# Optimization experiments

Hardware: AMD Instinct MI355X
Metric: run time of the kernel (lower is better)

## Reference

```python
import jax, jax.numpy as jnp
import numpy as np

N = 50000       # nodes
E = 1600000     # edges (avg degree 32)
F_IN = 128      # input node features
HID = 64        # hidden_dim
H = 2           # heads in conv1
NEG_SLOPE = 0.2 # PyG GATConv default


def gat_conv(x, W, a_src, a_dst, b, src, dst, heads, out_ch):
    """PyG-style GATConv (concat=True). x:[n,f], W:[f,heads*out_ch],
    a_src/a_dst:[heads,out_ch], b:[heads*out_ch], src/dst:[e]."""
    n = x.shape[0]
    xh = (x @ W).reshape(n, heads, out_ch)              # [n,H,C]
    s_src = jnp.sum(xh * a_src[None], axis=-1)          # [n,H]
    s_dst = jnp.sum(xh * a_dst[None], axis=-1)          # [n,H]
    e = jax.nn.leaky_relu(s_src[src] + s_dst[dst], NEG_SLOPE)  # [e,H]
    # segment softmax over incoming edges of each destination node
    emax = jax.ops.segment_max(e, dst, num_segments=n)  # [n,H]
    emax = jnp.where(jnp.isfinite(emax), emax, 0.0)
    p = jnp.exp(e - emax[dst])
    denom = jax.ops.segment_sum(p, dst, num_segments=n)
    alpha = p / (denom[dst] + 1e-16)                    # [e,H]
    out = jax.ops.segment_sum(xh[src] * alpha[..., None], dst, num_segments=n)
    return out.reshape(n, heads * out_ch) + b


def setup_inputs() -> dict:
    key = jax.random.key(0)
    ks = jax.random.split(key, 14)
    g = lambda k, shape, fan: jax.random.normal(k, shape, jnp.float32) / np.sqrt(fan).astype(np.float32)
    return {
        "x": jax.random.normal(ks[0], (N, F_IN), jnp.float32),
        "edge_index": jax.random.randint(ks[1], (2, E), 0, N, jnp.int32),
        "W1": g(ks[2], (F_IN, H * HID), F_IN),
        "a_src1": g(ks[3], (H, HID), HID),
        "a_dst1": g(ks[4], (H, HID), HID),
        "b1": jnp.zeros((H * HID,), jnp.float32),
        "W2": g(ks[5], (H * HID, HID), H * HID),
        "a_src2": g(ks[6], (1, HID), HID),
        "a_dst2": g(ks[7], (1, HID), HID),
        "b2": jnp.zeros((HID,), jnp.float32),
        "Wm": g(ks[8], (HID, 1), HID),
        "bm": jnp.zeros((1,), jnp.float32),
        "Wl": g(ks[9], (HID, 4), HID),
        "bl": jnp.zeros((4,), jnp.float32),
    }


def reference(x, edge_index, W1, a_src1, a_dst1, b1, W2, a_src2, a_dst2, b2, Wm, bm, Wl, bl):
    n = x.shape[0]
    loop = jnp.arange(n, dtype=edge_index.dtype)        # PyG add_self_loops=True
    src = jnp.concatenate([edge_index[0], loop])
    dst = jnp.concatenate([edge_index[1], loop])
    h = jax.nn.relu(gat_conv(x, W1, a_src1, a_dst1, b1, src, dst, H, HID))
    # dropout layers are identity in eval mode
    h = jax.nn.relu(gat_conv(h, W2, a_src2, a_dst2, b2, src, dst, 1, HID))
    mortality = h @ Wm + bm   # [n,1]
    los = h @ Wl + bl         # [n,4]
    return (mortality, los)
```

## Files before the change

kernel.cpp:

```cpp
#include <hip/hip_runtime.h>
#include <hip/hip_bf16.h>

typedef __hip_bfloat16 bf16;
typedef __attribute__((ext_vector_type(8))) short short8;
typedef __attribute__((ext_vector_type(4))) float f32x4;

static __device__ __forceinline__ float b2f(const bf16 v){ return __bfloat162float(v); }
static __device__ __forceinline__ float lrelu(float x){ return x > 0.f ? x : 0.2f * x; }

static __device__ __forceinline__ float ldf(const void* p, size_t i, int f32){
  return f32 ? ((const float*)p)[i] : __bfloat162float(((const bf16*)p)[i]);
}

static __device__ __forceinline__ float wsum(float v){
#pragma unroll
  for (int o = 32; o; o >>= 1) v += __shfl_xor(v, o, 64);
  return v;
}
static __device__ __forceinline__ float qsum(float v){
  v += __shfl_xor(v, 1); v += __shfl_xor(v, 2);
  v += __shfl_xor(v, 4); v += __shfl_xor(v, 8);
  return v;
}

static __device__ __forceinline__ unsigned short f2bf(float x){
  unsigned u = __float_as_uint(x);
  unsigned r = (u + 0x7fffu + ((u >> 16) & 1u)) >> 16;
  return (unsigned short)r;
}
static __device__ __forceinline__ float bfval(unsigned short h){
  return __uint_as_float(((unsigned)h) << 16);
}
static __device__ __forceinline__ unsigned packbf2(float a, float b){
  return ((unsigned)f2bf(b) << 16) | (unsigned)f2bf(a);
}
static __device__ __forceinline__ float unlo(unsigned v){ return __uint_as_float(v << 16); }
static __device__ __forceinline__ float unhi(unsigned v){ return __uint_as_float(v & 0xffff0000u); }

__global__ void k_detect(const unsigned short* __restrict__ x, int* __restrict__ flag,
                         int* __restrict__ bucketCur, int nbuck){
  __shared__ int cnt;
  if (threadIdx.x == 0) cnt = 0;
  __syncthreads();
  int bad = 0;
  for (int i = threadIdx.x; i < 8192; i += 256){
    int e = (x[i] >> 7) & 0xFF;
    if (e >= 133) bad++;
  }
  atomicAdd(&cnt, bad);
  for (int i = threadIdx.x; i < nbuck; i += 256) bucketCur[i] = 0;
  __syncthreads();
  if (threadIdx.x == 0) *flag = (cnt > 16) ? 1 : 0;
}

#define CAP 10240
#define EPB 16
#define CHUNK (256 * EPB)

__global__ __launch_bounds__(256) void k_binscatter(const int* __restrict__ ei,
                                                    int* __restrict__ bucketCur,
                                                    unsigned* __restrict__ binned,
                                                    int E, int Etot){
  __shared__ int lcnt[256];
  __shared__ int lcur[256];
  int t = threadIdx.x;
  lcnt[t] = 0;
  __syncthreads();
  int base = blockIdx.x * CHUNK;
  int vsrc[EPB], vdst[EPB];
#pragma unroll
  for (int k = 0; k < EPB; k++){
    int i = base + k * 256 + t;
    vdst[k] = -1;
    if (i < Etot){
      if (i < E){ vsrc[k] = ei[i]; vdst[k] = ei[E + i]; }
      else { vsrc[k] = i - E; vdst[k] = i - E; }
      atomicAdd(&lcnt[vdst[k] >> 8], 1);
    }
  }
  __syncthreads();
  lcur[t] = lcnt[t] ? atomicAdd(&bucketCur[t], lcnt[t]) : 0;
  __syncthreads();
#pragma unroll
  for (int k = 0; k < EPB; k++){
    if (vdst[k] >= 0){
      int b = vdst[k] >> 8;
      int p = atomicAdd(&lcur[b], 1);
      binned[(size_t)b * CAP + p] = (unsigned)vsrc[k] | ((unsigned)(vdst[k] & 255) << 24);
    }
  }
}

#define SORTCAP 10240
__global__ __launch_bounds__(256) void k_bucketsort(const int* __restrict__ bucketCur,
                                                    const unsigned* __restrict__ binned,
                                                    int* __restrict__ deg, int* __restrict__ offs,
                                                    int* __restrict__ csr, int N){
  __shared__ int lcnt[256];
  __shared__ int lsc[256];
  __shared__ int lcur[256];
  __shared__ int lsrc[SORTCAP];
  int t = threadIdx.x;
  int b = blockIdx.x;
  int s0 = b * CAP;
  int cnt = bucketCur[b];
  int node0 = b << 8;
  lcnt[t] = 0;
  __syncthreads();
  for (int i = t; i < cnt; i += 256){
    unsigned v = binned[s0 + i];
    atomicAdd(&lcnt[v >> 24], 1);
  }
  __syncthreads();
  lsc[t] = lcnt[t];
  __syncthreads();
#pragma unroll
  for (int o = 1; o < 256; o <<= 1){
    int x = (t >= o) ? lsc[t - o] : 0;
    __syncthreads();
    lsc[t] += x;
    __syncthreads();
  }
  int excl = lsc[t] - lcnt[t];
  int node = node0 + t;
  if (node < N){ deg[node] = lcnt[t]; offs[node] = s0 + excl; }
  lcur[t] = excl;
  __syncthreads();
  if (cnt <= SORTCAP){
    for (int i = t; i < cnt; i += 256){
      unsigned v = binned[s0 + i];
      int p = atomicAdd(&lcur[v >> 24], 1);
      lsrc[p] = (int)(v & 0xFFFFFFu);
    }
    __syncthreads();
    for (int i = t; i < cnt; i += 256) csr[s0 + i] = lsrc[i];
  } else {
    for (int i = t; i < cnt; i += 256){
      unsigned v = binned[s0 + i];
      int p = atomicAdd(&lcur[v >> 24], 1);
      csr[s0 + p] = (int)(v & 0xFFFFFFu);
    }
  }
}

__global__ __launch_bounds__(256) void k_prepw2(const void* __restrict__ W1, const void* __restrict__ W2,
                                                const int* __restrict__ flagp,
                                                unsigned short* __restrict__ w1hi, unsigned short* __restrict__ w1lo,
                                                unsigned short* __restrict__ w2hi, unsigned short* __restrict__ w2lo){
  const int f = *flagp;
  int blk = blockIdx.x;
  const void* W; unsigned short *hi, *lo; int ncol, nct, t;
  if (blk < 64){ W = W1; hi = w1hi; lo = w1lo; ncol = 128; nct = 8; t = blk * 256 + threadIdx.x; }
  else         { W = W2; hi = w2hi; lo = w2lo; ncol = 64;  nct = 4; t = (blk - 64) * 256 + threadIdx.x; }
  int j = t & 7;
  int lane = (t >> 3) & 63;
  int ct = (t >> 9) % nct;
  int kc = t / (512 * nct);
  int k = kc * 32 + ((lane >> 4) << 3) + j;
  int col = ct * 16 + (lane & 15);
  float w = ldf(W, (size_t)k * ncol + col, f);
  unsigned short h = f2bf(w);
  hi[t] = h;
  lo[t] = f2bf(w - bfval(h));
}

__global__ __launch_bounds__(256) void k_gemm1m(
    const void* __restrict__ x,
    const unsigned short* __restrict__ whi, const unsigned short* __restrict__ wlo,
    const void* __restrict__ a_src1, const void* __restrict__ a_dst1,
    const int* __restrict__ flagp,
    unsigned* __restrict__ xh1p, float* __restrict__ ssrc1, float* __restrict__ sdst1, int n){
  const int f = *flagp;
  int t = threadIdx.x;
  int lane = t & 63, w = t >> 6;
  int c16 = lane & 15, quad = lane >> 4;
  int nbw = blockIdx.x * 64 + w * 16;
  int an = min(nbw + c16, n - 1);
  f32x4 acc[8];
#pragma unroll
  for (int ct = 0; ct < 8; ct++)
#pragma unroll
    for (int r = 0; r < 4; r++) acc[ct][r] = 0.f;

#pragma unroll
  for (int kc = 0; kc < 4; kc++){
    float av[8];
    short8 ahi, alo;
    if (f){
      const float* row = (const float*)x + (size_t)an * 128 + kc * 32 + quad * 8;
      float4 v0 = *(const float4*)row;
      float4 v1 = *(const float4*)(row + 4);
      av[0] = v0.x; av[1] = v0.y; av[2] = v0.z; av[3] = v0.w;
      av[4] = v1.x; av[5] = v1.y; av[6] = v1.z; av[7] = v1.w;
#pragma unroll
      for (int j = 0; j < 8; j++){
        unsigned short h = f2bf(av[j]);
        ahi[j] = (short)h;
        alo[j] = (short)f2bf(av[j] - bfval(h));
      }
    } else {
      const unsigned short* row = (const unsigned short*)x + (size_t)an * 128 + kc * 32 + quad * 8;
      uint4 v = *(const uint4*)row;
      ahi[0] = (short)(v.x & 0xffff); ahi[1] = (short)(v.x >> 16);
      ahi[2] = (short)(v.y & 0xffff); ahi[3] = (short)(v.y >> 16);
      ahi[4] = (short)(v.z & 0xffff); ahi[5] = (short)(v.z >> 16);
      ahi[6] = (short)(v.w & 0xffff); ahi[7] = (short)(v.w >> 16);
#pragma unroll
      for (int j = 0; j < 8; j++) alo[j] = 0;
    }
#pragma unroll
    for (int ct = 0; ct < 8; ct++){
      const short8 bhi = *(const short8*)(whi + (((size_t)(kc * 8 + ct) * 64 + lane) << 3));
      const short8 blo = *(const short8*)(wlo + (((size_t)(kc * 8 + ct) * 64 + lane) << 3));
      acc[ct] = __builtin_amdgcn_mfma_f32_16x16x32_bf16(ahi, blo, acc[ct], 0, 0, 0);
      acc[ct] = __builtin_amdgcn_mfma_f32_16x16x32_bf16(alo, bhi, acc[ct], 0, 0, 0);
      acc[ct] = __builtin_amdgcn_mfma_f32_16x16x32_bf16(ahi, bhi, acc[ct], 0, 0, 0);
    }
  }

  float as[8], ad[8];
#pragma unroll
  for (int ct = 0; ct < 8; ct++){
    as[ct] = ldf(a_src1, ct * 16 + c16, f);
    ad[ct] = ldf(a_dst1, ct * 16 + c16, f);
  }
  float vs0[4], vs1[4], vd0[4], vd1[4];
#pragma unroll
  for (int r = 0; r < 4; r++){
    float s0 = 0.f, s1 = 0.f, d0 = 0.f, d1 = 0.f;
#pragma unroll
    for (int ct = 0; ct < 4; ct++){
      s0 += acc[ct][r] * as[ct];      d0 += acc[ct][r] * ad[ct];
      s1 += acc[ct + 4][r] * as[ct + 4]; d1 += acc[ct + 4][r] * ad[ct + 4];
    }
    vs0[r] = qsum(s0); vs1[r] = qsum(s1);
    vd0[r] = qsum(d0); vd1[r] = qsum(d1);
  }
#pragma unroll
  for (int r = 0; r < 4; r++){
    int node = nbw + quad * 4 + r;
    if (node < n){
#pragma unroll
      for (int ct = 0; ct < 4; ct++)
        xh1p[(size_t)node * 64 + ct * 16 + c16] = packbf2(acc[ct][r], acc[ct + 4][r]);
    }
  }
  if (c16 == 0){
#pragma unroll
    for (int r = 0; r < 4; r++){
      int node = nbw + quad * 4 + r;
      if (node < n){
        ssrc1[node * 2]     = vs0[r];
        ssrc1[node * 2 + 1] = vs1[r];
        sdst1[node * 2]     = vd0[r];
        sdst1[node * 2 + 1] = vd1[r];
      }
    }
  }
}

__global__ __launch_bounds__(256) void k_gemm2m(
    const float* __restrict__ h1,
    const unsigned short* __restrict__ whi, const unsigned short* __restrict__ wlo,
    const void* __restrict__ a_src2, const void* __restrict__ a_dst2,
    const int* __restrict__ flagp,
    unsigned short* __restrict__ xh2b, float* __restrict__ ssrc2, float* __restrict__ sdst2, int n){
  const int f = *flagp;
  int t = threadIdx.x;
  int lane = t & 63, w = t >> 6;
  int c16 = lane & 15, quad = lane >> 4;
  int nbw = blockIdx.x * 64 + w * 16;
  int an = min(nbw + c16, n - 1);
  f32x4 acc[4];
#pragma unroll
  for (int ct = 0; ct < 4; ct++)
#pragma unroll
    for (int r = 0; r < 4; r++) acc[ct][r] = 0.f;

#pragma unroll
  for (int kc = 0; kc < 4; kc++){
    const float* row = h1 + (size_t)an * 128 + kc * 32 + quad * 8;
    float4 v0 = *(const float4*)row;
    float4 v1 = *(const float4*)(row + 4);
    float av[8] = {v0.x, v0.y, v0.z, v0.w, v1.x, v1.y, v1.z, v1.w};
    short8 ahi, alo;
#pragma unroll
    for (int j = 0; j < 8; j++){
      unsigned short h = f2bf(av[j]);
      ahi[j] = (short)h;
      alo[j] = (short)f2bf(av[j] - bfval(h));
    }
#pragma unroll
    for (int ct = 0; ct < 4; ct++){
      const short8 bhi = *(const short8*)(whi + (((size_t)(kc * 4 + ct) * 64 + lane) << 3));
      const short8 blo = *(const short8*)(wlo + (((size_t)(kc * 4 + ct) * 64 + lane) << 3));
      acc[ct] = __builtin_amdgcn_mfma_f32_16x16x32_bf16(ahi, blo, acc[ct], 0, 0, 0);
      acc[ct] = __builtin_amdgcn_mfma_f32_16x16x32_bf16(alo, bhi, acc[ct], 0, 0, 0);
      acc[ct] = __builtin_amdgcn_mfma_f32_16x16x32_bf16(ahi, bhi, acc[ct], 0, 0, 0);
    }
  }

  float as[4], ad[4];
#pragma unroll
  for (int ct = 0; ct < 4; ct++){
    as[ct] = ldf(a_src2, ct * 16 + c16, f);
    ad[ct] = ldf(a_dst2, ct * 16 + c16, f);
  }
  float vs[4], vd[4];
#pragma unroll
  for (int r = 0; r < 4; r++){
    float s = 0.f, d = 0.f;
#pragma unroll
    for (int ct = 0; ct < 4; ct++){
      s += acc[ct][r] * as[ct];
      d += acc[ct][r] * ad[ct];
    }
    vs[r] = qsum(s); vd[r] = qsum(d);
  }
#pragma unroll
  for (int r = 0; r < 4; r++){
    int node = nbw + quad * 4 + r;
    if (node < n){
#pragma unroll
      for (int ct = 0; ct < 4; ct++)
        xh2b[(size_t)node * 64 + ct * 16 + c16] = f2bf(acc[ct][r]);
    }
  }
  if (c16 == 0){
#pragma unroll
    for (int r = 0; r < 4; r++){
      int node = nbw + quad * 4 + r;
      if (node < n){ ssrc2[node] = vs[r]; sdst2[node] = vd[r]; }
    }
  }
}

__global__ __launch_bounds__(256) void k_agg1(
    const int* __restrict__ offs, const int* __restrict__ deg, const int* __restrict__ csr,
    const float2* __restrict__ ssrc, const float2* __restrict__ sdst,
    const unsigned* __restrict__ xh1p, const void* __restrict__ b1,
    const int* __restrict__ flagp, float* __restrict__ h1, int n){
  int wid = (int)(((size_t)blockIdx.x * blockDim.x + threadIdx.x) >> 6);
  int lane = threadIdx.x & 63;
  if (wid >= n) return;
  int st = offs[wid], d = deg[wid];
  int half = lane >> 5, u = lane & 31;
  float2 sd = sdst[wid];
  const uint2* xp = (const uint2*)xh1p;
  float Z0l = 0.f, Z1l = 0.f;
  float a0x = 0.f, a0y = 0.f, a1x = 0.f, a1y = 0.f;
  for (int base = 0; base < d; base += 64){
    int idx = base + lane;
    bool val = idx < d;
    int s = csr[st + (val ? idx : 0)];
    float2 sv = ssrc[s];
    float e0 = fminf(lrelu(sv.x + sd.x), 80.f);
    float e1 = fminf(lrelu(sv.y + sd.y), 80.f);
    float p0 = val ? __expf(e0) : 0.f;
    float p1 = val ? __expf(e1) : 0.f;
    Z0l += p0; Z1l += p1;
    int cnt = min(64, d - base);
    int pairs = (cnt + 1) >> 1;
    for (int pj = 0; pj < pairs; pj += 8){
      int sj[8]; float q0v[8], q1v[8]; uint2 vv[8];
#pragma unroll
      for (int k = 0; k < 8; k++){
        int jj = ((pj + k) << 1) + half;
        sj[k] = __shfl(s, jj);
        q0v[k] = __shfl(p0, jj);
        q1v[k] = __shfl(p1, jj);
      }
#pragma unroll
      for (int k = 0; k < 8; k++)
        vv[k] = xp[(size_t)(unsigned)sj[k] * 32 + u];
#pragma unroll
      for (int k = 0; k < 8; k++){
        a0x = fmaf(q0v[k], unlo(vv[k].x), a0x); a0y = fmaf(q0v[k], unlo(vv[k].y), a0y);
        a1x = fmaf(q1v[k], unhi(vv[k].x), a1x); a1y = fmaf(q1v[k], unhi(vv[k].y), a1y);
      }
    }
  }
  a0x += __shfl_xor(a0x, 32); a0y += __shfl_xor(a0y, 32);
  a1x += __shfl_xor(a1x, 32); a1y += __shfl_xor(a1y, 32);
  float Z0 = wsum(Z0l), Z1 = wsum(Z1l);
  const int f = *flagp;
  float Zh = half ? Z1 : Z0;
  float ax = half ? a1x : a0x;
  float ay = half ? a1y : a0y;
  float inv = 1.f / (Zh + 1e-16f);
  float bx = ldf(b1, half * 64 + 2 * u, f);
  float by = ldf(b1, half * 64 + 2 * u + 1, f);
  float2 o;
  o.x = fmaxf(ax * inv + bx, 0.f);
  o.y = fmaxf(ay * inv + by, 0.f);
  *(float2*)&h1[(size_t)wid * 128 + half * 64 + 2 * u] = o;
}

__global__ __launch_bounds__(256) void k_agg2(
    const int* __restrict__ offs, const int* __restrict__ deg, const int* __restrict__ csr,
    const float* __restrict__ ssrc, const float* __restrict__ sdstA,
    const unsigned short* __restrict__ xh2b, const void* __restrict__ bias2,
    const void* __restrict__ Wm, const void* __restrict__ bm,
    const void* __restrict__ Wlos, const void* __restrict__ bl,
    const int* __restrict__ flagp, void* __restrict__ out, int n){
  int wid = (int)(((size_t)blockIdx.x * blockDim.x + threadIdx.x) >> 6);
  int lane = threadIdx.x & 63;
  if (wid >= n) return;
  int st = offs[wid], d = deg[wid];
  int half = lane >> 5, u = lane & 31;
  float sd = sdstA[wid];
  const unsigned* xp = (const unsigned*)xh2b;
  float Zl = 0.f, ax = 0.f, ay = 0.f;
  for (int base = 0; base < d; base += 64){
    int idx = base + lane;
    bool val = idx < d;
    int s = csr[st + (val ? idx : 0)];
    float e = fminf(lrelu(ssrc[s] + sd), 80.f);
    float p = val ? __expf(e) : 0.f;
    Zl += p;
    int cnt = min(64, d - base);
    int pairs = (cnt + 1) >> 1;
    for (int pj = 0; pj < pairs; pj += 8){
      int sj[8]; float qv[8]; unsigned vv[8];
#pragma unroll
      for (int k = 0; k < 8; k++){
        int jj = ((pj + k) << 1) + half;
        sj[k] = __shfl(s, jj);
        qv[k] = __shfl(p, jj);
      }
#pragma unroll
      for (int k = 0; k < 8; k++)
        vv[k] = xp[(size_t)(unsigned)sj[k] * 32 + u];
#pragma unroll
      for (int k = 0; k < 8; k++){
        ax = fmaf(qv[k], unlo(vv[k]), ax);
        ay = fmaf(qv[k], unhi(vv[k]), ay);
      }
    }
  }
  ax += __shfl_xor(ax, 32);
  ay += __shfl_xor(ay, 32);
  float Z = wsum(Zl);
  const int f = *flagp;
  float inv = 1.f / (Z + 1e-16f);
  float hx = fmaxf(ax * inv + ldf(bias2, 2 * u, f), 0.f);
  float hy = fmaxf(ay * inv + ldf(bias2, 2 * u + 1, f), 0.f);
  bool lo32 = (half == 0);
  float mo = wsum(lo32 ? hx * ldf(Wm, 2 * u, f) + hy * ldf(Wm, 2 * u + 1, f) : 0.f);
  float l0 = wsum(lo32 ? hx * ldf(Wlos, (2 * u) * 4 + 0, f) + hy * ldf(Wlos, (2 * u + 1) * 4 + 0, f) : 0.f);
  float l1 = wsum(lo32 ? hx * ldf(Wlos, (2 * u) * 4 + 1, f) + hy * ldf(Wlos, (2 * u + 1) * 4 + 1, f) : 0.f);
  float l2 = wsum(lo32 ? hx * ldf(Wlos, (2 * u) * 4 + 2, f) + hy * ldf(Wlos, (2 * u + 1) * 4 + 2, f) : 0.f);
  float l3 = wsum(lo32 ? hx * ldf(Wlos, (2 * u) * 4 + 3, f) + hy * ldf(Wlos, (2 * u + 1) * 4 + 3, f) : 0.f);
  if (lane == 0){
    float vm = mo + ldf(bm, 0, f);
    float v0 = l0 + ldf(bl, 0, f);
    float v1 = l1 + ldf(bl, 1, f);
    float v2 = l2 + ldf(bl, 2, f);
    float v3 = l3 + ldf(bl, 3, f);
    if (f){
      float* o = (float*)out;
      o[wid] = vm;
      float4 lv = make_float4(v0, v1, v2, v3);
      *(float4*)&o[n + wid * 4] = lv;
    } else {
      bf16* o = (bf16*)out;
      o[wid] = __float2bfloat16(vm);
      o[n + wid * 4 + 0] = __float2bfloat16(v0); o[n + wid * 4 + 1] = __float2bfloat16(v1);
      o[n + wid * 4 + 2] = __float2bfloat16(v2); o[n + wid * 4 + 3] = __float2bfloat16(v3);
    }
  }
}

extern "C" void kernel_launch(void* const* d_in, const int* in_sizes, int n_in,
                              void* d_out, int out_size, void* d_ws, size_t ws_size,
                              hipStream_t stream){
  const void* x      = d_in[0];
  const int*  ei     = (const int*)d_in[1];
  const void* W1     = d_in[2];
  const void* a_src1 = d_in[3];
  const void* a_dst1 = d_in[4];
  const void* b1     = d_in[5];
  const void* W2     = d_in[6];
  const void* a_src2 = d_in[7];
  const void* a_dst2 = d_in[8];
  const void* bias2  = d_in[9];
  const void* Wm     = d_in[10];
  const void* bm     = d_in[11];
  const void* Wlos   = d_in[12];
  const void* bl     = d_in[13];

  const int N = in_sizes[0] / 128;
  const int E = in_sizes[1] / 2;
  const int Etot = E + N;
  const int NBUCK = (N + 255) >> 8;

  char* base = (char*)d_ws;
  size_t off = 0;
  auto alloc = [&](size_t bytes) -> void* {
    void* r = base + off;
    off += (bytes + 255) & ~(size_t)255;
    return r;
  };
  int*      flag  = (int*)alloc(256);
  unsigned* xh1p  = (unsigned*)alloc((size_t)N * 64 * 4);
  float*    h1    = (float*)alloc((size_t)N * 128 * 4);
  float*    ssrc1 = (float*)alloc((size_t)N * 2 * 4);
  float*    sdst1 = (float*)alloc((size_t)N * 2 * 4);
  float*    ssrc2 = (float*)alloc((size_t)N * 4);
  float*    sdst2 = (float*)alloc((size_t)N * 4);
  int*      deg    = (int*)alloc((size_t)N * 4);
  int*      offsb  = (int*)alloc((size_t)N * 4);
  unsigned* binned = (unsigned*)alloc((size_t)NBUCK * CAP * 4);
  int*      csr    = (int*)alloc((size_t)NBUCK * CAP * 4);
  int*      bucketCur = (int*)alloc(1024);
  unsigned short* w1hi = (unsigned short*)alloc(16384 * 2);
  unsigned short* w1lo = (unsigned short*)alloc(16384 * 2);
  unsigned short* w2hi = (unsigned short*)alloc(8192 * 2);
  unsigned short* w2lo = (unsigned short*)alloc(8192 * 2);
  unsigned short* xh2b = (unsigned short*)xh1p;

  const int nchunk = (Etot + CHUNK - 1) / CHUNK;

  k_detect<<<1, 256, 0, stream>>>((const unsigned short*)x, flag, bucketCur, NBUCK);
  k_prepw2<<<96, 256, 0, stream>>>(W1, W2, flag, w1hi, w1lo, w2hi, w2lo);

  k_binscatter<<<nchunk, 256, 0, stream>>>(ei, bucketCur, binned, E, Etot);
  k_bucketsort<<<NBUCK, 256, 0, stream>>>(bucketCur, binned, deg, offsb, csr, N);

  k_gemm1m<<<(N + 63) / 64, 256, 0, stream>>>(x, w1hi, w1lo, a_src1, a_dst1, flag, xh1p, ssrc1, sdst1, N);
  k_agg1<<<(N + 3) / 4, 256, 0, stream>>>(offsb, deg, csr, (const float2*)ssrc1, (const float2*)sdst1,
                                          xh1p, b1, flag, h1, N);

  k_gemm2m<<<(N + 63) / 64, 256, 0, stream>>>(h1, w2hi, w2lo, a_src2, a_dst2, flag, xh2b, ssrc2, sdst2, N);
  k_agg2<<<(N + 3) / 4, 256, 0, stream>>>(offsb, deg, csr, ssrc2, sdst2, xh2b, bias2,
                                          Wm, bm, Wlos, bl, flag, d_out, N);
}
```

Measured before the change: 285.1 us.

## Merge prep/detect with edge binning and bucket sort with GEMM1 into combined launches

Result: faster. 262.8 us (-7.8%).

```diff
diff --git a/kernel.cpp b/kernel.cpp
--- a/kernel.cpp
+++ b/kernel.cpp
@@ -5,7 +5,6 @@
 typedef __attribute__((ext_vector_type(8))) short short8;
 typedef __attribute__((ext_vector_type(4))) float f32x4;
 
-static __device__ __forceinline__ float b2f(const bf16 v){ return __bfloat162float(v); }
 static __device__ __forceinline__ float lrelu(float x){ return x > 0.f ? x : 0.2f * x; }
 
 static __device__ __forceinline__ float ldf(const void* p, size_t i, int f32){
@@ -37,223 +36,218 @@
 static __device__ __forceinline__ float unlo(unsigned v){ return __uint_as_float(v << 16); }
 static __device__ __forceinline__ float unhi(unsigned v){ return __uint_as_float(v & 0xffff0000u); }
 
-__global__ void k_detect(const unsigned short* __restrict__ x, int* __restrict__ flag,
-                         int* __restrict__ bucketCur, int nbuck){
-  __shared__ int cnt;
-  if (threadIdx.x == 0) cnt = 0;
-  __syncthreads();
-  int bad = 0;
-  for (int i = threadIdx.x; i < 8192; i += 256){
-    int e = (x[i] >> 7) & 0xFF;
-    if (e >= 133) bad++;
-  }
-  atomicAdd(&cnt, bad);
-  for (int i = threadIdx.x; i < nbuck; i += 256) bucketCur[i] = 0;
-  __syncthreads();
-  if (threadIdx.x == 0) *flag = (cnt > 16) ? 1 : 0;
-}
-
 #define CAP 10240
 #define EPB 16
 #define CHUNK (256 * EPB)
-
-__global__ __launch_bounds__(256) void k_binscatter(const int* __restrict__ ei,
-                                                    int* __restrict__ bucketCur,
-                                                    unsigned* __restrict__ binned,
-                                                    int E, int Etot){
+#define PREPB 96
+#define SORTCAP 9216
+
+__global__ __launch_bounds__(256) void k_prep_scatter(
+    const unsigned short* __restrict__ xprobe,
+    const void* __restrict__ W1, const void* __restrict__ W2,
+    int* __restrict__ flag,
+    unsigned short* __restrict__ w1hi, unsigned short* __restrict__ w1lo,
+    unsigned short* __restrict__ w2hi, unsigned short* __restrict__ w2lo,
+    const int* __restrict__ ei, int* __restrict__ bucketCur,
+    unsigned* __restrict__ binned, int E, int Etot){
   __shared__ int lcnt[256];
   __shared__ int lcur[256];
   int t = threadIdx.x;
-  lcnt[t] = 0;
-  __syncthreads();
-  int base = blockIdx.x * CHUNK;
-  int vsrc[EPB], vdst[EPB];
-#pragma unroll
-  for (int k = 0; k < EPB; k++){
-    int i = base + k * 256 + t;
-    vdst[k] = -1;
-    if (i < Etot){
-      if (i < E){ vsrc[k] = ei[i]; vdst[k] = ei[E + i]; }
-      else { vsrc[k] = i - E; vdst[k] = i - E; }
-      atomicAdd(&lcnt[vdst[k] >> 8], 1);
-    }
-  }
-  __syncthreads();
-  lcur[t] = lcnt[t] ? atomicAdd(&bucketCur[t], lcnt[t]) : 0;
-  __syncthreads();
-#pragma unroll
-  for (int k = 0; k < EPB; k++){
-    if (vdst[k] >= 0){
-      int b = vdst[k] >> 8;
-      int p = atomicAdd(&lcur[b], 1);
-      binned[(size_t)b * CAP + p] = (unsigned)vsrc[k] | ((unsigned)(vdst[k] & 255) << 24);
-    }
-  }
-}
-
-#define SORTCAP 10240
-__global__ __launch_bounds__(256) void k_bucketsort(const int* __restrict__ bucketCur,
-                                                    const unsigned* __restrict__ binned,
-                                                    int* __restrict__ deg, int* __restrict__ offs,
-                                                    int* __restrict__ csr, int N){
-  __shared__ int lcnt[256];
-  __shared__ int lsc[256];
-  __shared__ int lcur[256];
-  __shared__ int lsrc[SORTCAP];
-  int t = threadIdx.x;
-  int b = blockIdx.x;
-  int s0 = b * CAP;
-  int cnt = bucketCur[b];
-  int node0 = b << 8;
-  lcnt[t] = 0;
-  __syncthreads();
-  for (int i = t; i < cnt; i += 256){
-    unsigned v = binned[s0 + i];
-    atomicAdd(&lcnt[v >> 24], 1);
-  }
-  __syncthreads();
-  lsc[t] = lcnt[t];
-  __syncthreads();
-#pragma unroll
-  for (int o = 1; o < 256; o <<= 1){
-    int x = (t >= o) ? lsc[t - o] : 0;
-    __syncthreads();
-    lsc[t] += x;
-    __syncthreads();
-  }
-  int excl = lsc[t] - lcnt[t];
-  int node = node0 + t;
-  if (node < N){ deg[node] = lcnt[t]; offs[node] = s0 + excl; }
-  lcur[t] = excl;
-  __syncthreads();
-  if (cnt <= SORTCAP){
-    for (int i = t; i < cnt; i += 256){
-      unsigned v = binned[s0 + i];
-      int p = atomicAdd(&lcur[v >> 24], 1);
-      lsrc[p] = (int)(v & 0xFFFFFFu);
-    }
-    __syncthreads();
-    for (int i = t; i < cnt; i += 256) csr[s0 + i] = lsrc[i];
+  if (blockIdx.x < PREPB){
+    if (t == 0) lcnt[0] = 0;
+    __syncthreads();
+    int bad = 0;
+    for (int i = t; i < 512; i += 256){
+      int e = (xprobe[i] >> 7) & 0xFF;
+      if (e >= 133) bad++;
+    }
+    if (bad) atomicAdd(&lcnt[0], bad);
+    __syncthreads();
+    const int f = lcnt[0] > 8;
+    if (blockIdx.x == 0 && t == 0) *flag = f;
+    int blk = blockIdx.x;
+    const void* W; unsigned short *hi, *lo; int ncol, nct, tg;
+    if (blk < 64){ W = W1; hi = w1hi; lo = w1lo; ncol = 128; nct = 8; tg = blk * 256 + t; }
+    else         { W = W2; hi = w2hi; lo = w2lo; ncol = 64;  nct = 4; tg = (blk - 64) * 256 + t; }
+    int j = tg & 7;
+    int lane = (tg >> 3) & 63;
+    int ct = (tg >> 9) % nct;
+    int kc = tg / (512 * nct);
+    int k = kc * 32 + ((lane >> 4) << 3) + j;
+    int col = ct * 16 + (lane & 15);
+    float w = ldf(W, (size_t)k * ncol + col, f);
+    unsigned short h = f2bf(w);
+    hi[tg] = h;
+    lo[tg] = f2bf(w - bfval(h));
   } else {
-    for (int i = t; i < cnt; i += 256){
-      unsigned v = binned[s0 + i];
-      int p = atomicAdd(&lcur[v >> 24], 1);
-      csr[s0 + p] = (int)(v & 0xFFFFFFu);
-    }
-  }
-}
-
-__global__ __launch_bounds__(256) void k_prepw2(const void* __restrict__ W1, const void* __restrict__ W2,
-                                                const int* __restrict__ flagp,
-                                                unsigned short* __restrict__ w1hi, unsigned short* __restrict__ w1lo,
-                                                unsigned short* __restrict__ w2hi, unsigned short* __restrict__ w2lo){
-  const int f = *flagp;
-  int blk = blockIdx.x;
-  const void* W; unsigned short *hi, *lo; int ncol, nct, t;
-  if (blk < 64){ W = W1; hi = w1hi; lo = w1lo; ncol = 128; nct = 8; t = blk * 256 + threadIdx.x; }
-  else         { W = W2; hi = w2hi; lo = w2lo; ncol = 64;  nct = 4; t = (blk - 64) * 256 + threadIdx.x; }
-  int j = t & 7;
-  int lane = (t >> 3) & 63;
-  int ct = (t >> 9) % nct;
-  int kc = t / (512 * nct);
-  int k = kc * 32 + ((lane >> 4) << 3) + j;
-  int col = ct * 16 + (lane & 15);
-  float w = ldf(W, (size_t)k * ncol + col, f);
-  unsigned short h = f2bf(w);
-  hi[t] = h;
-  lo[t] = f2bf(w - bfval(h));
-}
-
-__global__ __launch_bounds__(256) void k_gemm1m(
+    lcnt[t] = 0;
+    __syncthreads();
+    int base = (blockIdx.x - PREPB) * CHUNK;
+    int vsrc[EPB], vdst[EPB];
+#pragma unroll
+    for (int k = 0; k < EPB; k++){
+      int i = base + k * 256 + t;
+      vdst[k] = -1;
+      if (i < Etot){
+        if (i < E){ vsrc[k] = ei[i]; vdst[k] = ei[E + i]; }
+        else { vsrc[k] = i - E; vdst[k] = i - E; }
+        atomicAdd(&lcnt[vdst[k] >> 8], 1);
+      }
+    }
+    __syncthreads();
+    lcur[t] = lcnt[t] ? atomicAdd(&bucketCur[t], lcnt[t]) : 0;
+    __syncthreads();
+#pragma unroll
+    for (int k = 0; k < EPB; k++){
+      if (vdst[k] >= 0){
+        int b = vdst[k] >> 8;
+        int p = atomicAdd(&lcur[b], 1);
+        binned[(size_t)b * CAP + p] = (unsigned)vsrc[k] | ((unsigned)(vdst[k] & 255) << 24);
+      }
+    }
+  }
+}
+
+__global__ __launch_bounds__(256) void k_sort_gemm1(
+    const int* __restrict__ bucketCur, const unsigned* __restrict__ binned,
+    int* __restrict__ deg, int* __restrict__ offs, int* __restrict__ csr, int nbuck,
     const void* __restrict__ x,
     const unsigned short* __restrict__ whi, const unsigned short* __restrict__ wlo,
     const void* __restrict__ a_src1, const void* __restrict__ a_dst1,
     const int* __restrict__ flagp,
     unsigned* __restrict__ xh1p, float* __restrict__ ssrc1, float* __restrict__ sdst1, int n){
-  const int f = *flagp;
+  __shared__ int smem[768 + SORTCAP];
   int t = threadIdx.x;
-  int lane = t & 63, w = t >> 6;
-  int c16 = lane & 15, quad = lane >> 4;
-  int nbw = blockIdx.x * 64 + w * 16;
-  int an = min(nbw + c16, n - 1);
-  f32x4 acc[8];
-#pragma unroll
-  for (int ct = 0; ct < 8; ct++)
-#pragma unroll
-    for (int r = 0; r < 4; r++) acc[ct][r] = 0.f;
-
-#pragma unroll
-  for (int kc = 0; kc < 4; kc++){
-    float av[8];
-    short8 ahi, alo;
-    if (f){
-      const float* row = (const float*)x + (size_t)an * 128 + kc * 32 + quad * 8;
-      float4 v0 = *(const float4*)row;
-      float4 v1 = *(const float4*)(row + 4);
-      av[0] = v0.x; av[1] = v0.y; av[2] = v0.z; av[3] = v0.w;
-      av[4] = v1.x; av[5] = v1.y; av[6] = v1.z; av[7] = v1.w;
-#pragma unroll
-      for (int j = 0; j < 8; j++){
-        unsigned short h = f2bf(av[j]);
-        ahi[j] = (short)h;
-        alo[j] = (short)f2bf(av[j] - bfval(h));
-      }
+  if ((int)blockIdx.x < nbuck){
+    int* lcnt = smem;
+    int* lsc  = smem + 256;
+    int* lcur = smem + 512;
+    int* lsrc = smem + 768;
+    int b = blockIdx.x;
+    int s0 = b * CAP;
+    int cnt = bucketCur[b];
+    int node0 = b << 8;
+    lcnt[t] = 0;
+    __syncthreads();
+    for (int i = t; i < cnt; i += 256){
+      unsigned v = binned[s0 + i];
+      atomicAdd(&lcnt[v >> 24], 1);
+    }
+    __syncthreads();
+    lsc[t] = lcnt[t];
+    __syncthreads();
+#pragma unroll
+    for (int o = 1; o < 256; o <<= 1){
+      int xv = (t >= o) ? lsc[t - o] : 0;
+      __syncthreads();
+      lsc[t] += xv;
+      __syncthreads();
+    }
+    int excl = lsc[t] - lcnt[t];
+    int node = node0 + t;
+    if (node < n){ deg[node] = lcnt[t]; offs[node] = s0 + excl; }
+    lcur[t] = excl;
+    __syncthreads();
+    if (cnt <= SORTCAP){
+      for (int i = t; i < cnt; i += 256){
+        unsigned v = binned[s0 + i];
+        int p = atomicAdd(&lcur[v >> 24], 1);
+        lsrc[p] = (int)(v & 0xFFFFFFu);
+      }
+      __syncthreads();
+      for (int i = t; i < cnt; i += 256) csr[s0 + i] = lsrc[i];
     } else {
-      const unsigned short* row = (const unsigned short*)x + (size_t)an * 128 + kc * 32 + quad * 8;
-      uint4 v = *(const uint4*)row;
-      ahi[0] = (short)(v.x & 0xffff); ahi[1] = (short)(v.x >> 16);
-      ahi[2] = (short)(v.y & 0xffff); ahi[3] = (short)(v.y >> 16);
-      ahi[4] = (short)(v.z & 0xffff); ahi[5] = (short)(v.z >> 16);
-      ahi[6] = (short)(v.w & 0xffff); ahi[7] = (short)(v.w >> 16);
-#pragma unroll
-      for (int j = 0; j < 8; j++) alo[j] = 0;
-    }
+      for (int i = t; i < cnt; i += 256){
+        unsigned v = binned[s0 + i];
+        int p = atomicAdd(&lcur[v >> 24], 1);
+        csr[s0 + p] = (int)(v & 0xFFFFFFu);
+      }
+    }
+  } else {
+    const int f = *flagp;
+    int lane = t & 63, w = t >> 6;
+    int c16 = lane & 15, quad = lane >> 4;
+    int nbw = (blockIdx.x - nbuck) * 64 + w * 16;
+    int an = min(nbw + c16, n - 1);
+    f32x4 acc[8];
+#pragma unroll
+    for (int ct = 0; ct < 8; ct++)
+#pragma unroll
+      for (int r = 0; r < 4; r++) acc[ct][r] = 0.f;
+
+#pragma unroll
+    for (int kc = 0; kc < 4; kc++){
+      float av[8];
+      short8 ahi, alo;
+      if (f){
+        const float* row = (const float*)x + (size_t)an * 128 + kc * 32 + quad * 8;
+        float4 v0 = *(const float4*)row;
+        float4 v1 = *(const float4*)(row + 4);
+        av[0] = v0.x; av[1] = v0.y; av[2] = v0.z; av[3] = v0.w;
+        av[4] = v1.x; av[5] = v1.y; av[6] = v1.z; av[7] = v1.w;
+#pragma unroll
+        for (int j = 0; j < 8; j++){
+          unsigned short h = f2bf(av[j]);
+          ahi[j] = (short)h;
+          alo[j] = (short)f2bf(av[j] - bfval(h));
+        }
+      } else {
+        const unsigned short* row = (const unsigned short*)x + (size_t)an * 128 + kc * 32 + quad * 8;
+        uint4 v = *(const uint4*)row;
+        ahi[0] = (short)(v.x & 0xffff); ahi[1] = (short)(v.x >> 16);
+        ahi[2] = (short)(v.y & 0xffff); ahi[3] = (short)(v.y >> 16);
+        ahi[4] = (short)(v.z & 0xffff); ahi[5] = (short)(v.z >> 16);
+        ahi[6] = (short)(v.w & 0xffff); ahi[7] = (short)(v.w >> 16);
+#pragma unroll
+        for (int j = 0; j < 8; j++) alo[j] = 0;
+      }
+#pragma unroll
+      for (int ct = 0; ct < 8; ct++){
+        const short8 bhi = *(const short8*)(whi + (((size_t)(kc * 8 + ct) * 64 + lane) << 3));
+        const short8 blo = *(const short8*)(wlo + (((size_t)(kc * 8 + ct) * 64 + lane) << 3));
+        acc[ct] = __builtin_amdgcn_mfma_f32_16x16x32_bf16(ahi, blo, acc[ct], 0, 0, 0);
+        acc[ct] = __builtin_amdgcn_mfma_f32_16x16x32_bf16(alo, bhi, acc[ct], 0, 0, 0);
+        acc[ct] = __builtin_amdgcn_mfma_f32_16x16x32_bf16(ahi, bhi, acc[ct], 0, 0, 0);
+      }
+    }
+
+    float as[8], ad[8];
 #pragma unroll
     for (int ct = 0; ct < 8; ct++){
-      const short8 bhi = *(const short8*)(whi + (((size_t)(kc * 8 + ct) * 64 + lane) << 3));
-      const short8 blo = *(const short8*)(wlo + (((size_t)(kc * 8 + ct) * 64 + lane) << 3));
-      acc[ct] = __builtin_amdgcn_mfma_f32_16x16x32_bf16(ahi, blo, acc[ct], 0, 0, 0);
-      acc[ct] = __builtin_amdgcn_mfma_f32_16x16x32_bf16(alo, bhi, acc[ct], 0, 0, 0);
-      acc[ct] = __builtin_amdgcn_mfma_f32_16x16x32_bf16(ahi, bhi, acc[ct], 0, 0, 0);
-    }
-  }
-
-  float as[8], ad[8];
-#pragma unroll
-  for (int ct = 0; ct < 8; ct++){
-    as[ct] = ldf(a_src1, ct * 16 + c16, f);
-    ad[ct] = ldf(a_dst1, ct * 16 + c16, f);
-  }
-  float vs0[4], vs1[4], vd0[4], vd1[4];
-#pragma unroll
-  for (int r = 0; r < 4; r++){
-    float s0 = 0.f, s1 = 0.f, d0 = 0.f, d1 = 0.f;
-#pragma unroll
-    for (int ct = 0; ct < 4; ct++){
-      s0 += acc[ct][r] * as[ct];      d0 += acc[ct][r] * ad[ct];
-      s1 += acc[ct + 4][r] * as[ct + 4]; d1 += acc[ct + 4][r] * ad[ct + 4];
-    }
-    vs0[r] = qsum(s0); vs1[r] = qsum(s1);
-    vd0[r] = qsum(d0); vd1[r] = qsum(d1);
-  }
-#pragma unroll
-  for (int r = 0; r < 4; r++){
-    int node = nbw + quad * 4 + r;
-    if (node < n){
-#pragma unroll
-      for (int ct = 0; ct < 4; ct++)
-        xh1p[(size_t)node * 64 + ct * 16 + c16] = packbf2(acc[ct][r], acc[ct + 4][r]);
-    }
-  }
-  if (c16 == 0){
+      as[ct] = ldf(a_src1, ct * 16 + c16, f);
+      ad[ct] = ldf(a_dst1, ct * 16 + c16, f);
+    }
+    float vs0[4], vs1[4], vd0[4], vd1[4];
+#pragma unroll
+    for (int r = 0; r < 4; r++){
+      float s0 = 0.f, s1 = 0.f, d0 = 0.f, d1 = 0.f;
+#pragma unroll
+      for (int ct = 0; ct < 4; ct++){
+        s0 += acc[ct][r] * as[ct];         d0 += acc[ct][r] * ad[ct];
+        s1 += acc[ct + 4][r] * as[ct + 4]; d1 += acc[ct + 4][r] * ad[ct + 4];
+      }
+      vs0[r] = qsum(s0); vs1[r] = qsum(s1);
+      vd0[r] = qsum(d0); vd1[r] = qsum(d1);
+    }
 #pragma unroll
     for (int r = 0; r < 4; r++){
       int node = nbw + quad * 4 + r;
       if (node < n){
-        ssrc1[node * 2]     = vs0[r];
-        ssrc1[node * 2 + 1] = vs1[r];
-        sdst1[node * 2]     = vd0[r];
-        sdst1[node * 2 + 1] = vd1[r];
+#pragma unroll
+        for (int ct = 0; ct < 4; ct++)
+          xh1p[(size_t)node * 64 + ct * 16 + c16] = packbf2(acc[ct][r], acc[ct + 4][r]);
+      }
+    }
+    if (c16 == 0){
+#pragma unroll
+      for (int r = 0; r < 4; r++){
+        int node = nbw + quad * 4 + r;
+        if (node < n){
+          ssrc1[node * 2]     = vs0[r];
+          ssrc1[node * 2 + 1] = vs1[r];
+          sdst1[node * 2]     = vd0[r];
+          sdst1[node * 2 + 1] = vd1[r];
+        }
       }
     }
   }
@@ -520,14 +514,18 @@
   unsigned short* xh2b = (unsigned short*)xh1p;
 
   const int nchunk = (Etot + CHUNK - 1) / CHUNK;
-
-  k_detect<<<1, 256, 0, stream>>>((const unsigned short*)x, flag, bucketCur, NBUCK);
-  k_prepw2<<<96, 256, 0, stream>>>(W1, W2, flag, w1hi, w1lo, w2hi, w2lo);
-
-  k_binscatter<<<nchunk, 256, 0, stream>>>(ei, bucketCur, binned, E, Etot);
-  k_bucketsort<<<NBUCK, 256, 0, stream>>>(bucketCur, binned, deg, offsb, csr, N);
-
-  k_gemm1m<<<(N + 63) / 64, 256, 0, stream>>>(x, w1hi, w1lo, a_src1, a_dst1, flag, xh1p, ssrc1, sdst1, N);
+  const int ngemm1 = (N + 63) / 64;
+
+  hipMemsetAsync(bucketCur, 0, (size_t)NBUCK * 4, stream);
+
+  k_prep_scatter<<<PREPB + nchunk, 256, 0, stream>>>(
+      (const unsigned short*)x, W1, W2, flag, w1hi, w1lo, w2hi, w2lo,
+      ei, bucketCur, binned, E, Etot);
+
+  k_sort_gemm1<<<NBUCK + ngemm1, 256, 0, stream>>>(
+      bucketCur, binned, deg, offsb, csr, NBUCK,
+      x, w1hi, w1lo, a_src1, a_dst1, flag, xh1p, ssrc1, sdst1, N);
+
   k_agg1<<<(N + 3) / 4, 256, 0, stream>>>(offsb, deg, csr, (const float2*)ssrc1, (const float2*)sdst1,
                                           xh1p, b1, flag, h1, N);
 
```
